# Kernel tuning notes

Measured on AMD Instinct MI355X. Metric: run time of the kernel, lower is better.

## Reference

```python
import jax, jax.numpy as jnp
import numpy as np
from jax import lax


def setup_inputs() -> dict:
    key = jax.random.key(0)
    ks = jax.random.split(key, 9)
    B, C, H, W = 32, 16, 128, 128
    x = jax.random.normal(ks[0], (B, C, H, W), dtype=jnp.float32)
    # sobel_x kernel as in source; the executed code leaves conv_sobel_x with tiled sobel_x.T
    sobel = jnp.array([[-1.0, 0.0, 1.0], [-2.0, 0.0, 2.0], [-1.0, 0.0, 1.0]], dtype=jnp.float32) / 8.0
    Wx = jnp.tile(sobel.T, (16, 16, 1, 1))  # [O=16, I=16, 3, 3]
    bx = jax.random.normal(ks[1], (16,), dtype=jnp.float32) * 0.05
    # conv_sobel_y retained its default (random) init in the source; model as random params
    Wy = jax.random.normal(ks[2], (16, 16, 3, 3), dtype=jnp.float32) * (1.0 / np.sqrt(16 * 9))
    by = jax.random.normal(ks[3], (16,), dtype=jnp.float32) * 0.05
    W1 = jax.random.normal(ks[4], (128, 48), dtype=jnp.float32) * (1.0 / np.sqrt(48))
    b1 = jax.random.normal(ks[5], (128,), dtype=jnp.float32) * 0.01
    W2 = jax.random.normal(ks[6], (16, 128), dtype=jnp.float32) * (1.0 / np.sqrt(128))
    b2 = jax.random.normal(ks[7], (16,), dtype=jnp.float32) * 0.01
    return {"x": x, "Wx": Wx, "bx": bx, "Wy": Wy, "by": by,
            "W1": W1, "b1": b1, "W2": W2, "b2": b2}


def _conv_same(x, w, b):
    # x: [B,C,H,W], w: [O,I,3,3] -> [B,O,H,W]
    y = lax.conv_general_dilated(x, w, window_strides=(1, 1), padding="SAME",
                                 dimension_numbers=("NCHW", "OIHW", "NCHW"))
    return y + b[None, :, None, None]


def reference(x, Wx, bx, Wy, by, W1, b1, W2, b2):
    # concat along channels: [B, 48, H, W]
    feat = jnp.concatenate([_conv_same(x, Wx, bx), _conv_same(x, Wy, by), x], axis=1)
    # torch transpose(1, 3): [B, W, H, 48]
    feat = jnp.transpose(feat, (0, 3, 2, 1))
    h = jax.nn.relu(jnp.einsum("bwhc,oc->bwho", feat, W1) + b1)
    out = jnp.einsum("bwhc,oc->bwho", h, W2) + b2  # [B, W, H, 16]
    return out
```

## Files before the change

kernel.cpp:

```cpp
#include <hip/hip_runtime.h>
#include <hip/hip_bf16.h>

typedef __hip_bfloat16 bf16;
typedef __attribute__((ext_vector_type(8))) short short8;
typedef __attribute__((ext_vector_type(4))) short short4v;
typedef __attribute__((ext_vector_type(4))) float float4v;

#define HALO_H 18
#define HALO_W 10
#define CS 24
#define KS 136
#define XS_EL (HALO_W * HALO_H * CS)

#define W2B_EL 20480
#define WSF_BYTE 45056
#define XT_BYTE 65536

__device__ __forceinline__ unsigned int bfbits(float f) {
    bf16 h = __float2bfloat16(f);
    unsigned short u;
    __builtin_memcpy(&u, &h, 2);
    return (unsigned int)u;
}

__global__ void prep_all(const float* __restrict__ x,
                         const float* __restrict__ Wx, const float* __restrict__ bx,
                         const float* __restrict__ Wy, const float* __restrict__ by,
                         const float* __restrict__ W1, const float* __restrict__ b1,
                         const float* __restrict__ W2, const float* __restrict__ b2,
                         bf16* __restrict__ wsb, float* __restrict__ wsf,
                         bf16* __restrict__ xT, int tb) {
    int blk = blockIdx.x;
    int tid = threadIdx.x;
    if (blk < tb) {
        int b = blk >> 7;
        int w = tid >> 1, half = tid & 1;
        const float* src = x + (((size_t)(b * 16 + half * 8)) * 128 + (blk & 127)) * 128 + w;
        unsigned int pk[4];
#pragma unroll
        for (int i = 0; i < 4; ++i) {
            unsigned int lo = bfbits(src[(size_t)(2 * i) * 16384]);
            unsigned int hi = bfbits(src[(size_t)(2 * i + 1) * 16384]);
            pk[i] = lo | (hi << 16);
        }
        *(uint4*)(xT + ((size_t)blk * 128 + w) * 16 + half * 8) =
            make_uint4(pk[0], pk[1], pk[2], pk[3]);
        return;
    }
    int t = (blk - tb) * 256 + tid;
    int stride = 80 * 256;
    for (int f = t; f < 128 * 160; f += stride) {
        int j = f / 160, k = f - j * 160;
        int g = k >> 4, c = k & 15;
        float v = 0.0f;
        if (g < 9) {
            for (int o = 0; o < 16; ++o) {
                float wx = Wx[(o * 16 + c) * 9 + g];
                float wy = Wy[(o * 16 + c) * 9 + g];
                v = fmaf(W1[j * 48 + o], wx, v);
                v = fmaf(W1[j * 48 + 16 + o], wy, v);
            }
            if (g == 4) v += W1[j * 48 + 32 + c];
        }
        wsb[f] = __float2bfloat16(v);
    }
    for (int f = t; f < 2048; f += stride) wsb[W2B_EL + f] = __float2bfloat16(W2[f]);
    for (int j = t; j < 128; j += stride) {
        float v = b1[j];
        for (int o = 0; o < 16; ++o) {
            v = fmaf(W1[j * 48 + o], bx[o], v);
            v = fmaf(W1[j * 48 + 16 + o], by[o], v);
        }
        wsf[j] = v;
    }
    if (t < 16) wsf[128 + t] = b2[t];
}

__global__ __launch_bounds__(256, 2) void nca_mfma_t(const bf16* __restrict__ xT,
                                                     const bf16* __restrict__ wsb,
                                                     const float* __restrict__ wsf,
                                                     float* __restrict__ out,
                                                     int gridTiles) {
    __shared__ __align__(16) bf16 xs[2][XS_EL];
    __shared__ __align__(16) bf16 hs[128 * KS];

    const int tid = threadIdx.x;
    const int wave = tid >> 6;
    const int lane = tid & 63;
    const int hl = lane & 15;
    const int quad = lane >> 4;
    const int r0 = quad * 4;
    const int mgrp = wave >> 1;
    const int ngrp = wave & 1;

    short8 afrag[4][5];
#pragma unroll
    for (int mt = 0; mt < 4; ++mt) {
        int m = mgrp * 64 + mt * 16 + hl;
#pragma unroll
        for (int q = 0; q < 5; ++q)
            afrag[mt][q] = *(const short8*)(wsb + m * 160 + q * 32 + quad * 8);
    }
    short8 w2frag[4];
#pragma unroll
    for (int r = 0; r < 4; ++r)
        w2frag[r] = *(const short8*)(wsb + W2B_EL + hl * 128 + r * 32 + quad * 8);
    float b1r[4][4];
#pragma unroll
    for (int mt = 0; mt < 4; ++mt)
#pragma unroll
        for (int r = 0; r < 4; ++r) b1r[mt][r] = wsf[mgrp * 64 + mt * 16 + r0 + r];
    float b2r[4];
#pragma unroll
    for (int r = 0; r < 4; ++r) b2r[r] = wsf[128 + r0 + r];

    const int hh0 = tid / 20, rr0 = tid % 20;
    const int sww0 = rr0 >> 1, shf0 = rr0 & 1;
    const int f1 = tid + 256;
    const int hh1 = f1 / 20, rr1 = f1 % 20;
    const int sww1 = rr1 >> 1, shf1 = rr1 & 1;
    const bool has1 = (tid < 104);

    uint4 pre0, pre1;

#define LOAD_TILE(T)                                                                  \
    {                                                                                 \
        int b_ = (T) >> 7, rem_ = (T) & 127;                                          \
        int w0_ = (rem_ >> 3) * 8, h0_ = (rem_ & 7) * 16;                             \
        {                                                                             \
            int gh = h0_ - 1 + hh0, gw = w0_ - 1 + sww0;                              \
            bool ok = ((unsigned)gh < 128u) && ((unsigned)gw < 128u);                 \
            long off = (((long)b_ << 14) + gh * 128 + gw) * 16 + (shf0 << 3);         \
            const uint4* p = (const uint4*)(xT + (ok ? off : 0));                     \
            uint4 v = *p;                                                             \
            if (!ok) { v.x = 0; v.y = 0; v.z = 0; v.w = 0; }                          \
            pre0 = v;                                                                 \
        }                                                                             \
        if (has1) {                                                                   \
            int gh = h0_ - 1 + hh1, gw = w0_ - 1 + sww1;                              \
            bool ok = ((unsigned)gh < 128u) && ((unsigned)gw < 128u);                 \
            long off = (((long)b_ << 14) + gh * 128 + gw) * 16 + (shf1 << 3);         \
            const uint4* p = (const uint4*)(xT + (ok ? off : 0));                     \
            uint4 v = *p;                                                             \
            if (!ok) { v.x = 0; v.y = 0; v.z = 0; v.w = 0; }                          \
            pre1 = v;                                                                 \
        }                                                                             \
    }

    int t = blockIdx.x;
    LOAD_TILE(t);
    int buf = 0;

    for (; t < 4096; t += gridTiles) {
        const int b = t >> 7;
        const int rem = t & 127;
        const int w0 = (rem >> 3) * 8;
        const int h0 = (rem & 7) * 16;

        *(uint4*)(&xs[buf][(sww0 * HALO_H + hh0) * CS + shf0 * 8]) = pre0;
        if (has1) *(uint4*)(&xs[buf][(sww1 * HALO_H + hh1) * CS + shf1 * 8]) = pre1;
        __syncthreads();

        int tn = t + gridTiles;
        if (tn < 4096) LOAD_TILE(tn);

        float4v acc[4][4];
#pragma unroll
        for (int mt = 0; mt < 4; ++mt)
#pragma unroll
            for (int nt = 0; nt < 4; ++nt) acc[mt][nt] = (float4v)0.0f;

#pragma unroll
        for (int q = 0; q < 5; ++q) {
            int g = q * 2 + (quad >> 1);
            if (g > 8) g = 8;
            int kh = g / 3, kw = g - kh * 3;
            int c0 = (quad & 1) * 8;
            short8 bfrag[4];
#pragma unroll
            for (int nt = 0; nt < 4; ++nt) {
                int ww = ngrp * 4 + nt + kw;
                bfrag[nt] = *(const short8*)(&xs[buf][(ww * HALO_H + hl + kh) * CS + c0]);
            }
#pragma unroll
            for (int nt = 0; nt < 4; ++nt)
#pragma unroll
                for (int mt = 0; mt < 4; ++mt)
                    acc[mt][nt] = __builtin_amdgcn_mfma_f32_16x16x32_bf16(
                        afrag[mt][q], bfrag[nt], acc[mt][nt], 0, 0, 0);
        }

#pragma unroll
        for (int mt = 0; mt < 4; ++mt)
#pragma unroll
            for (int nt = 0; nt < 4; ++nt) {
                int p = (ngrp * 4 + nt) * 16 + hl;
                int m = mgrp * 64 + mt * 16 + r0;
                short4v pk;
#pragma unroll
                for (int r = 0; r < 4; ++r) {
                    float v = acc[mt][nt][r] + b1r[mt][r];
                    v = fmaxf(v, 0.0f);
                    bf16 hb = __float2bfloat16(v);
                    pk[r] = *reinterpret_cast<short*>(&hb);
                }
                *(short4v*)(hs + p * KS + m) = pk;
            }
        __syncthreads();

        float4v acc2[2];
        acc2[0] = (float4v)0.0f;
        acc2[1] = (float4v)0.0f;
#pragma unroll
        for (int r = 0; r < 4; ++r) {
#pragma unroll
            for (int i = 0; i < 2; ++i) {
                int p = (wave * 2 + i) * 16 + hl;
                short8 bfrag = *(const short8*)(hs + p * KS + r * 32 + quad * 8);
                acc2[i] = __builtin_amdgcn_mfma_f32_16x16x32_bf16(
                    w2frag[r], bfrag, acc2[i], 0, 0, 0);
            }
        }

#pragma unroll
        for (int i = 0; i < 2; ++i) {
            int nt = wave * 2 + i;
            size_t ofs = (((size_t)b * 128 + (w0 + nt)) * 128 + (h0 + hl)) * 16 + r0;
            float4 v = make_float4(acc2[i][0] + b2r[0], acc2[i][1] + b2r[1],
                                   acc2[i][2] + b2r[2], acc2[i][3] + b2r[3]);
            *(float4*)(out + ofs) = v;
        }
        buf ^= 1;
    }
#undef LOAD_TILE
}

__global__ __launch_bounds__(256, 2) void nca_mfma_fb(const float* __restrict__ x,
                                                      const bf16* __restrict__ wsb,
                                                      const float* __restrict__ wsf,
                                                      float* __restrict__ out,
                                                      int gridTiles) {
    __shared__ bf16 xs[HALO_W * HALO_H * CS];
    __shared__ bf16 hs[128 * KS];

    const int tid = threadIdx.x;
    const int wave = tid >> 6;
    const int lane = tid & 63;
    const int hl = lane & 15;
    const int quad = lane >> 4;
    const int r0 = quad * 4;
    const int mgrp = wave >> 1;
    const int ngrp = wave & 1;

    short8 afrag[4][5];
#pragma unroll
    for (int mt = 0; mt < 4; ++mt) {
        int m = mgrp * 64 + mt * 16 + hl;
#pragma unroll
        for (int q = 0; q < 5; ++q)
            afrag[mt][q] = *(const short8*)(wsb + m * 160 + q * 32 + quad * 8);
    }
    short8 w2frag[4];
#pragma unroll
    for (int r = 0; r < 4; ++r)
        w2frag[r] = *(const short8*)(wsb + W2B_EL + hl * 128 + r * 32 + quad * 8);
    float b1r[4][4];
#pragma unroll
    for (int mt = 0; mt < 4; ++mt)
#pragma unroll
        for (int r = 0; r < 4; ++r) b1r[mt][r] = wsf[mgrp * 64 + mt * 16 + r0 + r];
    float b2r[4];
#pragma unroll
    for (int r = 0; r < 4; ++r) b2r[r] = wsf[128 + r0 + r];

    for (int t = blockIdx.x; t < 4096; t += gridTiles) {
        int b = t >> 7;
        int rem = t & 127;
        int wt = rem >> 3, ht = rem & 7;
        int h0 = ht * 16, w0 = wt * 8;

        __syncthreads();

        const float* xb = x + (size_t)b * 16 * 128 * 128;
        for (int f = tid; f < 16 * HALO_H * HALO_W; f += 256) {
            int c = f / (HALO_H * HALO_W);
            int rr = f - c * (HALO_H * HALO_W);
            int hh = rr / HALO_W;
            int ww = rr - hh * HALO_W;
            int gh = h0 - 1 + hh, gw = w0 - 1 + ww;
            float v = 0.0f;
            if ((unsigned)gh < 128u && (unsigned)gw < 128u)
                v = xb[(c * 128 + gh) * 128 + gw];
            xs[(ww * HALO_H + hh) * CS + c] = __float2bfloat16(v);
        }
        __syncthreads();

        float4v acc[4][4];
#pragma unroll
        for (int mt = 0; mt < 4; ++mt)
#pragma unroll
            for (int nt = 0; nt < 4; ++nt) acc[mt][nt] = (float4v)0.0f;

#pragma unroll
        for (int q = 0; q < 5; ++q) {
            int g = q * 2 + (quad >> 1);
            if (g > 8) g = 8;
            int kh = g / 3, kw = g - kh * 3;
            int c0 = (quad & 1) * 8;
            short8 bfrag[4];
#pragma unroll
            for (int nt = 0; nt < 4; ++nt) {
                int ww = ngrp * 4 + nt + kw;
                bfrag[nt] = *(const short8*)(xs + (ww * HALO_H + hl + kh) * CS + c0);
            }
#pragma unroll
            for (int nt = 0; nt < 4; ++nt)
#pragma unroll
                for (int mt = 0; mt < 4; ++mt)
                    acc[mt][nt] = __builtin_amdgcn_mfma_f32_16x16x32_bf16(
                        afrag[mt][q], bfrag[nt], acc[mt][nt], 0, 0, 0);
        }

#pragma unroll
        for (int mt = 0; mt < 4; ++mt)
#pragma unroll
            for (int nt = 0; nt < 4; ++nt) {
                int p = (ngrp * 4 + nt) * 16 + hl;
                int m = mgrp * 64 + mt * 16 + r0;
                short4v pk;
#pragma unroll
                for (int r = 0; r < 4; ++r) {
                    float v = acc[mt][nt][r] + b1r[mt][r];
                    v = fmaxf(v, 0.0f);
                    bf16 hb = __float2bfloat16(v);
                    pk[r] = *reinterpret_cast<short*>(&hb);
                }
                *(short4v*)(hs + p * KS + m) = pk;
            }
        __syncthreads();

        float4v acc2[2];
        acc2[0] = (float4v)0.0f;
        acc2[1] = (float4v)0.0f;
#pragma unroll
        for (int r = 0; r < 4; ++r) {
#pragma unroll
            for (int i = 0; i < 2; ++i) {
                int p = (wave * 2 + i) * 16 + hl;
                short8 bfrag = *(const short8*)(hs + p * KS + r * 32 + quad * 8);
                acc2[i] = __builtin_amdgcn_mfma_f32_16x16x32_bf16(
                    w2frag[r], bfrag, acc2[i], 0, 0, 0);
            }
        }

#pragma unroll
        for (int i = 0; i < 2; ++i) {
            int nt = wave * 2 + i;
            size_t ofs = (((size_t)b * 128 + (w0 + nt)) * 128 + (h0 + hl)) * 16 + r0;
            float4 v = make_float4(acc2[i][0] + b2r[0], acc2[i][1] + b2r[1],
                                   acc2[i][2] + b2r[2], acc2[i][3] + b2r[3]);
            *(float4*)(out + ofs) = v;
        }
    }
}

extern "C" void kernel_launch(void* const* d_in, const int* in_sizes, int n_in,
                              void* d_out, int out_size, void* d_ws, size_t ws_size,
                              hipStream_t stream) {
    const float* x  = (const float*)d_in[0];
    const float* Wx = (const float*)d_in[1];
    const float* bx = (const float*)d_in[2];
    const float* Wy = (const float*)d_in[3];
    const float* by = (const float*)d_in[4];
    const float* W1 = (const float*)d_in[5];
    const float* b1 = (const float*)d_in[6];
    const float* W2 = (const float*)d_in[7];
    const float* b2 = (const float*)d_in[8];
    bf16* wsb = (bf16*)d_ws;
    float* wsf = (float*)((char*)d_ws + WSF_BYTE);
    bf16* xT = (bf16*)((char*)d_ws + XT_BYTE);
    float* out = (float*)d_out;

    const size_t need = (size_t)XT_BYTE + (size_t)32 * 128 * 128 * 16 * 2;
    const bool big = ws_size >= need;
    const int tb = big ? 4096 : 0;

    hipLaunchKernelGGL(prep_all, dim3(tb + 80), dim3(256), 0, stream,
                       x, Wx, bx, Wy, by, W1, b1, W2, b2, wsb, wsf, xT, tb);
    if (big) {
        const int grid = 512;
        hipLaunchKernelGGL(nca_mfma_t, dim3(grid), dim3(256), 0, stream,
                           xT, wsb, wsf, out, grid);
    } else {
        const int grid = 1024;
        hipLaunchKernelGGL(nca_mfma_fb, dim3(grid), dim3(256), 0, stream,
                           x, wsb, wsf, out, grid);
    }
}
```

Baseline: 124.1 us.

## Give each wave group a private halo slice and double-buffer hidden activations

The shared input tile and its barrier are replaced by per-column-group halo slices (6 columns each). Each wave writes every element it later reads, so the barrier after the halo store can be dropped. The hidden-activation buffer is double-buffered so the next tile's first stage can overlap the previous tile's second stage with only one barrier per tile. In exchange, overlapping halo columns are loaded twice (more global and LDS traffic), and LDS use grows to about 80KB per block.

```diff
diff --git a/kernel.cpp b/kernel.cpp
--- a/kernel.cpp
+++ b/kernel.cpp
@@ -10,7 +10,9 @@
 #define HALO_W 10
 #define CS 24
 #define KS 136
-#define XS_EL (HALO_W * HALO_H * CS)
+#define XS_W 6
+#define XS_REG (XS_W * HALO_H * CS)
+#define HS_EL (128 * KS)
 
 #define W2B_EL 20480
 #define WSF_BYTE 45056
@@ -81,8 +83,8 @@
                                                      const float* __restrict__ wsf,
                                                      float* __restrict__ out,
                                                      int gridTiles) {
-    __shared__ __align__(16) bf16 xs[2][XS_EL];
-    __shared__ __align__(16) bf16 hs[128 * KS];
+    __shared__ __align__(16) bf16 xs[2][XS_REG];
+    __shared__ __align__(16) bf16 hs[2][HS_EL];
 
     const int tid = threadIdx.x;
     const int wave = tid >> 6;
@@ -114,42 +116,40 @@
 #pragma unroll
     for (int r = 0; r < 4; ++r) b2r[r] = wsf[128 + r0 + r];
 
-    const int hh0 = tid / 20, rr0 = tid % 20;
-    const int sww0 = rr0 >> 1, shf0 = rr0 & 1;
-    const int f1 = tid + 256;
-    const int hh1 = f1 / 20, rr1 = f1 % 20;
-    const int sww1 = rr1 >> 1, shf1 = rr1 & 1;
-    const bool has1 = (tid < 104);
-
-    uint4 pre0, pre1;
+    int sc_lds[4], sc_row[4], sc_col[4], sc_cf[4];
+#pragma unroll
+    for (int s = 0; s < 4; ++s) {
+        int u = lane + 64 * s;
+        int pos = u >> 1, cf = u & 1;
+        int col = pos / HALO_H, row = pos - col * HALO_H;
+        sc_lds[s] = ngrp * XS_REG + (col * HALO_H + row) * CS + cf * 8;
+        sc_row[s] = row; sc_col[s] = col; sc_cf[s] = cf;
+    }
+    const bool has3 = (lane < 24);
+
+    uint4 pre[4];
+    bf16* xsf = (bf16*)xs;
 
 #define LOAD_TILE(T)                                                                  \
     {                                                                                 \
         int b_ = (T) >> 7, rem_ = (T) & 127;                                          \
         int w0_ = (rem_ >> 3) * 8, h0_ = (rem_ & 7) * 16;                             \
-        {                                                                             \
-            int gh = h0_ - 1 + hh0, gw = w0_ - 1 + sww0;                              \
-            bool ok = ((unsigned)gh < 128u) && ((unsigned)gw < 128u);                 \
-            long off = (((long)b_ << 14) + gh * 128 + gw) * 16 + (shf0 << 3);         \
+        _Pragma("unroll")                                                             \
+        for (int s = 0; s < 4; ++s) {                                                 \
+            int gh = h0_ - 1 + sc_row[s];                                             \
+            int gw = w0_ - 1 + ngrp * 4 + sc_col[s];                                  \
+            bool ok = (s < 3 || has3) && ((unsigned)gh < 128u) && ((unsigned)gw < 128u); \
+            long off = (((long)b_ << 14) + gh * 128 + gw) * 16 + (sc_cf[s] << 3);     \
             const uint4* p = (const uint4*)(xT + (ok ? off : 0));                     \
             uint4 v = *p;                                                             \
             if (!ok) { v.x = 0; v.y = 0; v.z = 0; v.w = 0; }                          \
-            pre0 = v;                                                                 \
-        }                                                                             \
-        if (has1) {                                                                   \
-            int gh = h0_ - 1 + hh1, gw = w0_ - 1 + sww1;                              \
-            bool ok = ((unsigned)gh < 128u) && ((unsigned)gw < 128u);                 \
-            long off = (((long)b_ << 14) + gh * 128 + gw) * 16 + (shf1 << 3);         \
-            const uint4* p = (const uint4*)(xT + (ok ? off : 0));                     \
-            uint4 v = *p;                                                             \
-            if (!ok) { v.x = 0; v.y = 0; v.z = 0; v.w = 0; }                          \
-            pre1 = v;                                                                 \
+            pre[s] = v;                                                               \
         }                                                                             \
     }
 
     int t = blockIdx.x;
     LOAD_TILE(t);
-    int buf = 0;
+    int tb = 0;
 
     for (; t < 4096; t += gridTiles) {
         const int b = t >> 7;
@@ -157,9 +157,10 @@
         const int w0 = (rem >> 3) * 8;
         const int h0 = (rem & 7) * 16;
 
-        *(uint4*)(&xs[buf][(sww0 * HALO_H + hh0) * CS + shf0 * 8]) = pre0;
-        if (has1) *(uint4*)(&xs[buf][(sww1 * HALO_H + hh1) * CS + shf1 * 8]) = pre1;
-        __syncthreads();
+#pragma unroll
+        for (int s = 0; s < 3; ++s)
+            *(uint4*)(xsf + sc_lds[s]) = pre[s];
+        if (has3) *(uint4*)(xsf + sc_lds[3]) = pre[3];
 
         int tn = t + gridTiles;
         if (tn < 4096) LOAD_TILE(tn);
@@ -170,6 +171,7 @@
 #pragma unroll
             for (int nt = 0; nt < 4; ++nt) acc[mt][nt] = (float4v)0.0f;
 
+        const bf16* xw = xsf + ngrp * XS_REG;
 #pragma unroll
         for (int q = 0; q < 5; ++q) {
             int g = q * 2 + (quad >> 1);
@@ -178,10 +180,8 @@
             int c0 = (quad & 1) * 8;
             short8 bfrag[4];
 #pragma unroll
-            for (int nt = 0; nt < 4; ++nt) {
-                int ww = ngrp * 4 + nt + kw;
-                bfrag[nt] = *(const short8*)(&xs[buf][(ww * HALO_H + hl + kh) * CS + c0]);
-            }
+            for (int nt = 0; nt < 4; ++nt)
+                bfrag[nt] = *(const short8*)(xw + ((nt + kw) * HALO_H + hl + kh) * CS + c0);
 #pragma unroll
             for (int nt = 0; nt < 4; ++nt)
 #pragma unroll
@@ -190,6 +190,7 @@
                         afrag[mt][q], bfrag[nt], acc[mt][nt], 0, 0, 0);
         }
 
+        bf16* hsw = (bf16*)hs + tb * HS_EL;
 #pragma unroll
         for (int mt = 0; mt < 4; ++mt)
 #pragma unroll
@@ -204,7 +205,7 @@
                     bf16 hb = __float2bfloat16(v);
                     pk[r] = *reinterpret_cast<short*>(&hb);
                 }
-                *(short4v*)(hs + p * KS + m) = pk;
+                *(short4v*)(hsw + p * KS + m) = pk;
             }
         __syncthreads();
 
@@ -216,7 +217,7 @@
 #pragma unroll
             for (int i = 0; i < 2; ++i) {
                 int p = (wave * 2 + i) * 16 + hl;
-                short8 bfrag = *(const short8*)(hs + p * KS + r * 32 + quad * 8);
+                short8 bfrag = *(const short8*)(hsw + p * KS + r * 32 + quad * 8);
                 acc2[i] = __builtin_amdgcn_mfma_f32_16x16x32_bf16(
                     w2frag[r], bfrag, acc2[i], 0, 0, 0);
             }
@@ -230,7 +231,7 @@
                                    acc2[i][2] + b2r[2], acc2[i][3] + b2r[3]);
             *(float4*)(out + ofs) = v;
         }
-        buf ^= 1;
+        tb ^= 1;
     }
 #undef LOAD_TILE
 }
@@ -240,8 +241,8 @@
                                                       const float* __restrict__ wsf,
                                                       float* __restrict__ out,
                                                       int gridTiles) {
-    __shared__ bf16 xs[HALO_W * HALO_H * CS];
-    __shared__ bf16 hs[128 * KS];
+    __shared__ bf16 xsb[HALO_W * HALO_H * CS];
+    __shared__ bf16 hsb[128 * KS];
 
     const int tid = threadIdx.x;
     const int wave = tid >> 6;
@@ -291,7 +292,7 @@
             float v = 0.0f;
             if ((unsigned)gh < 128u && (unsigned)gw < 128u)
                 v = xb[(c * 128 + gh) * 128 + gw];
-            xs[(ww * HALO_H + hh) * CS + c] = __float2bfloat16(v);
+            xsb[(ww * HALO_H + hh) * CS + c] = __float2bfloat16(v);
         }
         __syncthreads();
 
@@ -311,7 +312,7 @@
 #pragma unroll
             for (int nt = 0; nt < 4; ++nt) {
                 int ww = ngrp * 4 + nt + kw;
-                bfrag[nt] = *(const short8*)(xs + (ww * HALO_H + hl + kh) * CS + c0);
+                bfrag[nt] = *(const short8*)(xsb + (ww * HALO_H + hl + kh) * CS + c0);
             }
 #pragma unroll
             for (int nt = 0; nt < 4; ++nt)
@@ -335,7 +336,7 @@
                     bf16 hb = __float2bfloat16(v);
                     pk[r] = *reinterpret_cast<short*>(&hb);
                 }
-                *(short4v*)(hs + p * KS + m) = pk;
+                *(short4v*)(hsb + p * KS + m) = pk;
             }
         __syncthreads();
 
@@ -347,7 +348,7 @@
 #pragma unroll
             for (int i = 0; i < 2; ++i) {
                 int p = (wave * 2 + i) * 16 + hl;
-                short8 bfrag = *(const short8*)(hs + p * KS + r * 32 + quad * 8);
+                short8 bfrag = *(const short8*)(hsb + p * KS + r * 32 + quad * 8);
                 acc2[i] = __builtin_amdgcn_mfma_f32_16x16x32_bf16(
                     w2frag[r], bfrag, acc2[i], 0, 0, 0);
             }
```

Result: slower. 141.6 us (+14.1%).
